# Optimization experiments

Hardware: AMD Instinct MI355X
Metric: run time of the kernel (lower is better)

Reference implementation:

```python
import jax, jax.numpy as jnp
import numpy as np


def _pixel_unshuffle(y, r=2):
    # torch.nn.PixelUnshuffle: out[:, c*r*r + i*r + j, h, w] = in[:, c, h*r+i, w*r+j]
    B, C, H, W = y.shape
    y = y.reshape(B, C, H // r, r, W // r, r)
    y = y.transpose(0, 1, 3, 5, 2, 4)  # (B, C, r, r, H//r, W//r)
    return y.reshape(B, C * r * r, H // r, W // r)


def setup_inputs() -> dict:
    key = jax.random.key(0)
    kx, kw = jax.random.split(key)
    n_feat = 96
    x = jax.random.normal(kx, (8, n_feat, 256, 256), dtype=jnp.float32)
    # conv weight: (out=n_feat//2, in=n_feat, 3, 3), kaiming-ish scale
    fan_in = n_feat * 3 * 3
    W = jax.random.normal(kw, (n_feat // 2, n_feat, 3, 3), dtype=jnp.float32) * (1.0 / np.sqrt(fan_in))
    return {"x": x, "W": W}


def reference(x, W):
    # 3x3 conv, stride 1, padding 1, no bias (FP32 path of QConv2ds)
    y = jax.lax.conv_general_dilated(
        x, W,
        window_strides=(1, 1),
        padding=((1, 1), (1, 1)),
        dimension_numbers=("NCHW", "OIHW", "NCHW"),
    )
    # PixelUnshuffle(2): [B, C/2, H, W] -> [B, 2C, H/2, W/2]
    return _pixel_unshuffle(y, r=2)
```

## Files before the change

kernel.cpp:

```cpp
#include <hip/hip_runtime.h>


typedef __attribute__((ext_vector_type(8))) short bf16x8;
typedef __attribute__((ext_vector_type(4))) float f32x4;
typedef __attribute__((ext_vector_type(4))) unsigned uint4v;

#define CIN 96
#define COUT 48
#define HW 256
#define TH 8
#define TW 32
#define HALO_H (TH + 2)
#define HALO_W (TW + 2)
#define NPIX (HALO_H * HALO_W)
#define CC 32
#define CIPAD 40

static __device__ __forceinline__ unsigned bfbits(float f) {
    unsigned u = __builtin_bit_cast(unsigned, f);
    return (u + 0x7fffu + ((u >> 16) & 1u)) >> 16;
}
static __device__ __forceinline__ unsigned packbf(float lo, float hi) {
    return (bfbits(lo) & 0xffffu) | (bfbits(hi) << 16);
}

__global__ __launch_bounds__(256) void wtransform(
    const float* __restrict__ Wg, short* __restrict__ blob)
{
    int t = blockIdx.x * 256 + threadIdx.x;
    if (t >= COUT * CIN * 9) return;
    int co  = t / (CIN * 9);
    int rem = t - co * (CIN * 9);
    int ci  = rem / 9;
    int d   = rem - ci * 9;
    int cc  = ci >> 5, cl = ci & 31;
    int ct  = co >> 4;
    int lane = (co & 15) | ((cl >> 3) << 4);
    int j   = cl & 7;
    blob[((((cc * 9 + d) * 3 + ct) * 64 + lane) * 8) + j] = (short)bfbits(Wg[t]);
}

__global__ __launch_bounds__(256, 4) void conv3x3_unshuffle_mfma(
    const float* __restrict__ x,
    const short* __restrict__ wblob,
    float* __restrict__ out)
{
    __shared__ short xs[NPIX * CIPAD];

    const int tid  = threadIdx.x;
    const int lane = tid & 63;
    const int wv   = tid >> 6;
    const int b    = blockIdx.z;
    const int h0   = blockIdx.y * TH;
    const int w0   = blockIdx.x * TW;

    const float* xb = x + (size_t)b * CIN * HW * HW;

    f32x4 acc[4][3];
#pragma unroll
    for (int pt = 0; pt < 4; ++pt)
#pragma unroll
        for (int ct = 0; ct < 3; ++ct)
            acc[pt][ct] = (f32x4){0.f, 0.f, 0.f, 0.f};

    for (int cc = 0; cc < CIN / CC; ++cc) {
        constexpr int TASKS = 4 * NPIX;
        for (int t = tid; t < TASKS; t += 256) {
            int cig = t / NPIX;
            int p   = t - cig * NPIX;
            int r   = p / HALO_W;
            int c   = p - r * HALO_W;
            int gh  = h0 + r - 1;
            int gw  = w0 + c - 1;
            float v[8];
#pragma unroll
            for (int j = 0; j < 8; ++j) v[j] = 0.f;
            if (((unsigned)gh < HW) & ((unsigned)gw < HW)) {
                const float* src = xb + (size_t)(cc * CC + cig * 8) * HW * HW + gh * HW + gw;
#pragma unroll
                for (int j = 0; j < 8; ++j) v[j] = src[(size_t)j * HW * HW];
            }
            uint4v pk;
            pk.x = packbf(v[0], v[1]);
            pk.y = packbf(v[2], v[3]);
            pk.z = packbf(v[4], v[5]);
            pk.w = packbf(v[6], v[7]);
            *(uint4v*)&xs[p * CIPAD + cig * 8] = pk;
        }
        __syncthreads();

        const short* wc = wblob + (size_t)cc * 9 * 3 * 512;
        bf16x8 afc[3];
#pragma unroll
        for (int ct = 0; ct < 3; ++ct)
            afc[ct] = *(const bf16x8*)(wc + ct * 512 + lane * 8);

#pragma unroll
        for (int d = 0; d < 9; ++d) {
            bf16x8 afn[3];
            if (d < 8) {
#pragma unroll
                for (int ct = 0; ct < 3; ++ct)
                    afn[ct] = *(const bf16x8*)(wc + ((d + 1) * 3 + ct) * 512 + lane * 8);
            }
            const int dy = d / 3, dx = d - 3 * (d / 3);
            bf16x8 bfv[4];
#pragma unroll
            for (int pt = 0; pt < 4; ++pt) {
                int hr = 2 * wv + (pt >> 1) + dy;
                int hc = (pt & 1) * 16 + (lane & 15) + dx;
                bfv[pt] = *(const bf16x8*)&xs[(hr * HALO_W + hc) * CIPAD + (lane >> 4) * 8];
            }
#pragma unroll
            for (int pt = 0; pt < 4; ++pt)
#pragma unroll
                for (int ct = 0; ct < 3; ++ct)
                    acc[pt][ct] = __builtin_amdgcn_mfma_f32_16x16x32_bf16(
                        afc[ct], bfv[pt], acc[pt][ct], 0, 0, 0);
#pragma unroll
            for (int ct = 0; ct < 3; ++ct) afc[ct] = afn[ct];
        }
        __syncthreads();
    }

#pragma unroll
    for (int pt = 0; pt < 4; ++pt) {
        int oh = h0 + 2 * wv + (pt >> 1);
        int ow = w0 + (pt & 1) * 16 + (lane & 15);
        int sub = ((oh & 1) << 1) | (ow & 1);
        size_t pixoff = (size_t)(oh >> 1) * (HW / 2) + (ow >> 1);
#pragma unroll
        for (int ct = 0; ct < 3; ++ct) {
#pragma unroll
            for (int e = 0; e < 4; ++e) {
                int co = ct * 16 + (lane >> 4) * 4 + e;
                out[((size_t)b * (COUT * 4) + co * 4 + sub) * (HW / 2) * (HW / 2) + pixoff] =
                    acc[pt][ct][e];
            }
        }
    }
}

extern "C" void kernel_launch(void* const* d_in, const int* in_sizes, int n_in,
                              void* d_out, int out_size, void* d_ws, size_t ws_size,
                              hipStream_t stream) {
    const float* x  = (const float*)d_in[0];
    const float* Wg = (const float*)d_in[1];
    float* out      = (float*)d_out;
    short* blob     = (short*)d_ws;

    wtransform<<<(COUT * CIN * 9 + 255) / 256, 256, 0, stream>>>(Wg, blob);

    dim3 grid(HW / TW, HW / TH, 8);
    conv3x3_unshuffle_mfma<<<grid, dim3(256), 0, stream>>>(x, blob, out);
}
```

Before: 356.9 us.

## Prefetch next input channel chunk into registers while computing current chunk

Splits the shared-memory staging into an issue phase (global loads into a per-thread register buffer) and a commit phase (bf16 pack and LDS store). The next channel chunk's loads are issued before the MFMA loop over the current chunk, hiding global memory latency behind compute. It also uses the HIP bf16x2 conversion intrinsic for packing, prefetches weights across chunk boundaries, lowers the occupancy hint from 4 to 3 blocks to make room for the 48-float register buffer, and writes outputs with nontemporal stores. Costs are higher register pressure and an extra barrier per chunk.

```diff
diff --git a/kernel.cpp b/kernel.cpp
--- a/kernel.cpp
+++ b/kernel.cpp
@@ -1,4 +1,5 @@
 #include <hip/hip_runtime.h>
+#include <hip/hip_bf16.h>
 
 
 typedef __attribute__((ext_vector_type(8))) short bf16x8;
@@ -15,13 +16,18 @@
 #define NPIX (HALO_H * HALO_W)
 #define CC 32
 #define CIPAD 40
+#define TASKS (4 * NPIX)
+#define NT 6
 
 static __device__ __forceinline__ unsigned bfbits(float f) {
     unsigned u = __builtin_bit_cast(unsigned, f);
     return (u + 0x7fffu + ((u >> 16) & 1u)) >> 16;
 }
 static __device__ __forceinline__ unsigned packbf(float lo, float hi) {
-    return (bfbits(lo) & 0xffffu) | (bfbits(hi) << 16);
+    __hip_bfloat162 h = __float22bfloat162_rn(float2{lo, hi});
+    unsigned r;
+    __builtin_memcpy(&r, &h, sizeof(r));
+    return r;
 }
 
 __global__ __launch_bounds__(256) void wtransform(
@@ -40,7 +46,7 @@
     blob[((((cc * 9 + d) * 3 + ct) * 64 + lane) * 8) + j] = (short)bfbits(Wg[t]);
 }
 
-__global__ __launch_bounds__(256, 4) void conv3x3_unshuffle_mfma(
+__global__ __launch_bounds__(256, 3) void conv3x3_unshuffle_mfma(
     const float* __restrict__ x,
     const short* __restrict__ wblob,
     float* __restrict__ out)
@@ -56,6 +62,54 @@
 
     const float* xb = x + (size_t)b * CIN * HW * HW;
 
+    int loff[NT];
+#pragma unroll
+    for (int k = 0; k < NT; ++k) {
+        int t = tid + k * 256;
+        if (t < TASKS) {
+            int cig = t / NPIX;
+            int p   = t - cig * NPIX;
+            loff[k] = p * CIPAD + cig * 8;
+        } else loff[k] = -1;
+    }
+
+    float vbuf[NT][8];
+
+    auto stage_issue = [&](int cc) {
+#pragma unroll
+        for (int k = 0; k < NT; ++k) {
+            int t   = tid + k * 256;
+            int cig = t / NPIX;
+            int p   = t - cig * NPIX;
+            int r   = p / HALO_W;
+            int c   = p - r * HALO_W;
+            int gh  = h0 + r - 1;
+            int gw  = w0 + c - 1;
+            bool inb = (t < TASKS) & ((unsigned)gh < HW) & ((unsigned)gw < HW);
+            if (inb) {
+                const float* src = xb + (size_t)(cc * CC + cig * 8) * HW * HW + gh * HW + gw;
+#pragma unroll
+                for (int j = 0; j < 8; ++j) vbuf[k][j] = src[(size_t)j * HW * HW];
+            } else {
+#pragma unroll
+                for (int j = 0; j < 8; ++j) vbuf[k][j] = 0.f;
+            }
+        }
+    };
+    auto stage_commit = [&]() {
+#pragma unroll
+        for (int k = 0; k < NT; ++k) {
+            if (loff[k] >= 0) {
+                uint4v pk;
+                pk.x = packbf(vbuf[k][0], vbuf[k][1]);
+                pk.y = packbf(vbuf[k][2], vbuf[k][3]);
+                pk.z = packbf(vbuf[k][4], vbuf[k][5]);
+                pk.w = packbf(vbuf[k][6], vbuf[k][7]);
+                *(uint4v*)&xs[loff[k]] = pk;
+            }
+        }
+    };
+
     f32x4 acc[4][3];
 #pragma unroll
     for (int pt = 0; pt < 4; ++pt)
@@ -63,46 +117,30 @@
         for (int ct = 0; ct < 3; ++ct)
             acc[pt][ct] = (f32x4){0.f, 0.f, 0.f, 0.f};
 
+    stage_issue(0);
+    stage_commit();
+
+    bf16x8 afc[3];
+#pragma unroll
+    for (int ct = 0; ct < 3; ++ct)
+        afc[ct] = *(const bf16x8*)(wblob + ct * 512 + lane * 8);
+
+    __syncthreads();
+
     for (int cc = 0; cc < CIN / CC; ++cc) {
-        constexpr int TASKS = 4 * NPIX;
-        for (int t = tid; t < TASKS; t += 256) {
-            int cig = t / NPIX;
-            int p   = t - cig * NPIX;
-            int r   = p / HALO_W;
-            int c   = p - r * HALO_W;
-            int gh  = h0 + r - 1;
-            int gw  = w0 + c - 1;
-            float v[8];
-#pragma unroll
-            for (int j = 0; j < 8; ++j) v[j] = 0.f;
-            if (((unsigned)gh < HW) & ((unsigned)gw < HW)) {
-                const float* src = xb + (size_t)(cc * CC + cig * 8) * HW * HW + gh * HW + gw;
-#pragma unroll
-                for (int j = 0; j < 8; ++j) v[j] = src[(size_t)j * HW * HW];
-            }
-            uint4v pk;
-            pk.x = packbf(v[0], v[1]);
-            pk.y = packbf(v[2], v[3]);
-            pk.z = packbf(v[4], v[5]);
-            pk.w = packbf(v[6], v[7]);
-            *(uint4v*)&xs[p * CIPAD + cig * 8] = pk;
-        }
-        __syncthreads();
+        if (cc < 2) stage_issue(cc + 1);
 
         const short* wc = wblob + (size_t)cc * 9 * 3 * 512;
-        bf16x8 afc[3];
-#pragma unroll
-        for (int ct = 0; ct < 3; ++ct)
-            afc[ct] = *(const bf16x8*)(wc + ct * 512 + lane * 8);
 
 #pragma unroll
         for (int d = 0; d < 9; ++d) {
+            const short* wn = (d < 8) ? (wc + (d + 1) * 3 * 512)
+                                      : (cc < 2 ? wc + 9 * 3 * 512 : wc);
             bf16x8 afn[3];
-            if (d < 8) {
 #pragma unroll
-                for (int ct = 0; ct < 3; ++ct)
-                    afn[ct] = *(const bf16x8*)(wc + ((d + 1) * 3 + ct) * 512 + lane * 8);
-            }
+            for (int ct = 0; ct < 3; ++ct)
+                afn[ct] = *(const bf16x8*)(wn + ct * 512 + lane * 8);
+
             const int dy = d / 3, dx = d - 3 * (d / 3);
             bf16x8 bfv[4];
 #pragma unroll
@@ -120,7 +158,12 @@
 #pragma unroll
             for (int ct = 0; ct < 3; ++ct) afc[ct] = afn[ct];
         }
+
         __syncthreads();
+        if (cc < 2) {
+            stage_commit();
+            __syncthreads();
+        }
     }
 
 #pragma unroll
@@ -134,8 +177,8 @@
 #pragma unroll
             for (int e = 0; e < 4; ++e) {
                 int co = ct * 16 + (lane >> 4) * 4 + e;
-                out[((size_t)b * (COUT * 4) + co * 4 + sub) * (HW / 2) * (HW / 2) + pixoff] =
-                    acc[pt][ct][e];
+                __builtin_nontemporal_store(acc[pt][ct][e],
+                    &out[((size_t)b * (COUT * 4) + co * 4 + sub) * (HW / 2) * (HW / 2) + pixoff]);
             }
         }
     }
```

Result: slower. 404.7 us (+13.4%).

## Give each wave a private 4x16 halo tile and drop block barriers

Applied to the files above, without the earlier changes.

Each wave now stages its own 4x16 output tile's halo in a private LDS slice. This removes both __syncthreads per channel chunk, but neighbouring waves now load overlapping halo rows redundantly. The grid is flattened to 2048 blocks with a swizzled block-to-tile mapping, which changes how tiles are spread across XCDs. Weight fragments are prefetched across chunk boundaries, and bf16 packing now uses the HIP intrinsic. The trade is more halo global loads (6x18 per 4x16 versus 10x34 per 8x32) and a larger LDS footprint, in exchange for no cross-wave synchronisation.

```diff
diff --git a/kernel.cpp b/kernel.cpp
--- a/kernel.cpp
+++ b/kernel.cpp
@@ -1,4 +1,5 @@
 #include <hip/hip_runtime.h>
+#include <hip/hip_bf16.h>
 
 
 typedef __attribute__((ext_vector_type(8))) short bf16x8;
@@ -8,11 +9,11 @@
 #define CIN 96
 #define COUT 48
 #define HW 256
-#define TH 8
-#define TW 32
-#define HALO_H (TH + 2)
-#define HALO_W (TW + 2)
-#define NPIX (HALO_H * HALO_W)
+#define WTH 4
+#define WTW 16
+#define WHH (WTH + 2)
+#define WHW (WTW + 2)
+#define WNP (WHH * WHW)
 #define CC 32
 #define CIPAD 40
 
@@ -21,7 +22,10 @@
     return (u + 0x7fffu + ((u >> 16) & 1u)) >> 16;
 }
 static __device__ __forceinline__ unsigned packbf(float lo, float hi) {
-    return (bfbits(lo) & 0xffffu) | (bfbits(hi) << 16);
+    __hip_bfloat162 h = __float22bfloat162_rn(float2{lo, hi});
+    unsigned r;
+    __builtin_memcpy(&r, &h, sizeof(r));
+    return r;
 }
 
 __global__ __launch_bounds__(256) void wtransform(
@@ -45,74 +49,86 @@
     const short* __restrict__ wblob,
     float* __restrict__ out)
 {
-    __shared__ short xs[NPIX * CIPAD];
+    __shared__ short xs[4][WNP * CIPAD];
 
     const int tid  = threadIdx.x;
     const int lane = tid & 63;
     const int wv   = tid >> 6;
-    const int b    = blockIdx.z;
-    const int h0   = blockIdx.y * TH;
-    const int w0   = blockIdx.x * TW;
+
+    int bid = blockIdx.x;
+    int nid = (bid & 7) * 256 + (bid >> 3);
+    int b   = nid >> 8;
+    int ty  = (nid >> 4) & 15;
+    int tx  = nid & 15;
+    int h0  = ty * 16 + wv * WTH;
+    int w0  = tx * 16;
 
     const float* xb = x + (size_t)b * CIN * HW * HW;
+    short* xw = xs[wv];
 
-    f32x4 acc[4][3];
+    f32x4 acc[WTH][3];
 #pragma unroll
-    for (int pt = 0; pt < 4; ++pt)
+    for (int pt = 0; pt < WTH; ++pt)
 #pragma unroll
         for (int ct = 0; ct < 3; ++ct)
             acc[pt][ct] = (f32x4){0.f, 0.f, 0.f, 0.f};
 
+    bf16x8 afc[3];
+#pragma unroll
+    for (int ct = 0; ct < 3; ++ct)
+        afc[ct] = *(const bf16x8*)(wblob + ct * 512 + lane * 8);
+
     for (int cc = 0; cc < CIN / CC; ++cc) {
-        constexpr int TASKS = 4 * NPIX;
-        for (int t = tid; t < TASKS; t += 256) {
-            int cig = t / NPIX;
-            int p   = t - cig * NPIX;
-            int r   = p / HALO_W;
-            int c   = p - r * HALO_W;
-            int gh  = h0 + r - 1;
-            int gw  = w0 + c - 1;
-            float v[8];
 #pragma unroll
-            for (int j = 0; j < 8; ++j) v[j] = 0.f;
-            if (((unsigned)gh < HW) & ((unsigned)gw < HW)) {
-                const float* src = xb + (size_t)(cc * CC + cig * 8) * HW * HW + gh * HW + gw;
+        for (int cig = 0; cig < 4; ++cig) {
 #pragma unroll
-                for (int j = 0; j < 8; ++j) v[j] = src[(size_t)j * HW * HW];
+            for (int rep = 0; rep < 2; ++rep) {
+                int p = lane + rep * 64;
+                bool act = p < WNP;
+                int r = p / WHW;
+                int c = p - r * WHW;
+                int gh = h0 + r - 1;
+                int gw = w0 + c - 1;
+                float v[8];
+#pragma unroll
+                for (int j = 0; j < 8; ++j) v[j] = 0.f;
+                if (act & ((unsigned)gh < HW) & ((unsigned)gw < HW)) {
+                    const float* src = xb + (size_t)(cc * CC + cig * 8) * HW * HW
+                                          + gh * HW + gw;
+#pragma unroll
+                    for (int j = 0; j < 8; ++j) v[j] = src[(size_t)j * HW * HW];
+                }
+                if (act) {
+                    uint4v pk;
+                    pk.x = packbf(v[0], v[1]);
+                    pk.y = packbf(v[2], v[3]);
+                    pk.z = packbf(v[4], v[5]);
+                    pk.w = packbf(v[6], v[7]);
+                    *(uint4v*)&xw[p * CIPAD + cig * 8] = pk;
+                }
             }
-            uint4v pk;
-            pk.x = packbf(v[0], v[1]);
-            pk.y = packbf(v[2], v[3]);
-            pk.z = packbf(v[4], v[5]);
-            pk.w = packbf(v[6], v[7]);
-            *(uint4v*)&xs[p * CIPAD + cig * 8] = pk;
         }
-        __syncthreads();
 
         const short* wc = wblob + (size_t)cc * 9 * 3 * 512;
-        bf16x8 afc[3];
-#pragma unroll
-        for (int ct = 0; ct < 3; ++ct)
-            afc[ct] = *(const bf16x8*)(wc + ct * 512 + lane * 8);
-
 #pragma unroll
         for (int d = 0; d < 9; ++d) {
+            const short* wn = (d < 8) ? (wc + (d + 1) * 3 * 512)
+                                      : (cc < 2 ? wc + 9 * 3 * 512 : wc);
             bf16x8 afn[3];
-            if (d < 8) {
 #pragma unroll
-                for (int ct = 0; ct < 3; ++ct)
-                    afn[ct] = *(const bf16x8*)(wc + ((d + 1) * 3 + ct) * 512 + lane * 8);
-            }
+            for (int ct = 0; ct < 3; ++ct)
+                afn[ct] = *(const bf16x8*)(wn + ct * 512 + lane * 8);
+
             const int dy = d / 3, dx = d - 3 * (d / 3);
-            bf16x8 bfv[4];
+            bf16x8 bfv[WTH];
 #pragma unroll
-            for (int pt = 0; pt < 4; ++pt) {
-                int hr = 2 * wv + (pt >> 1) + dy;
-                int hc = (pt & 1) * 16 + (lane & 15) + dx;
-                bfv[pt] = *(const bf16x8*)&xs[(hr * HALO_W + hc) * CIPAD + (lane >> 4) * 8];
+            for (int pt = 0; pt < WTH; ++pt) {
+                int hr = pt + dy;
+                int hc = (lane & 15) + dx;
+                bfv[pt] = *(const bf16x8*)&xw[(hr * WHW + hc) * CIPAD + (lane >> 4) * 8];
             }
 #pragma unroll
-            for (int pt = 0; pt < 4; ++pt)
+            for (int pt = 0; pt < WTH; ++pt)
 #pragma unroll
                 for (int ct = 0; ct < 3; ++ct)
                     acc[pt][ct] = __builtin_amdgcn_mfma_f32_16x16x32_bf16(
@@ -120,13 +136,12 @@
 #pragma unroll
             for (int ct = 0; ct < 3; ++ct) afc[ct] = afn[ct];
         }
-        __syncthreads();
     }
 
 #pragma unroll
-    for (int pt = 0; pt < 4; ++pt) {
-        int oh = h0 + 2 * wv + (pt >> 1);
-        int ow = w0 + (pt & 1) * 16 + (lane & 15);
+    for (int pt = 0; pt < WTH; ++pt) {
+        int oh = h0 + pt;
+        int ow = w0 + (lane & 15);
         int sub = ((oh & 1) << 1) | (ow & 1);
         size_t pixoff = (size_t)(oh >> 1) * (HW / 2) + (ow >> 1);
 #pragma unroll
@@ -151,6 +166,5 @@
 
     wtransform<<<(COUT * CIN * 9 + 255) / 256, 256, 0, stream>>>(Wg, blob);
 
-    dim3 grid(HW / TW, HW / TH, 8);
-    conv3x3_unshuffle_mfma<<<grid, dim3(256), 0, stream>>>(x, blob, out);
+    conv3x3_unshuffle_mfma<<<dim3(2048), dim3(256), 0, stream>>>(x, blob, out);
 }
```

New measurement: 388.6 us. 8.9% more time.
